# Kernel tuning notes

Hardware: AMD Instinct MI355X
Metric: run time of the kernel (lower is better)

The kernel has to match this reference:

```python
import jax, jax.numpy as jnp
import numpy as np

QMAX = 127.0  # torch.iinfo(torch.int8).max


def setup_inputs() -> dict:
    key = jax.random.key(0)
    k1, k2 = jax.random.split(key)
    input_act = jax.random.normal(k1, (4, 2048, 4096), dtype=jnp.float32)
    # nn.Linear weight: [out_features, in_features], fp weights pre-quantization
    weight = jax.random.normal(k2, (4096, 4096), dtype=jnp.float32) * 0.02
    return {"input_act": input_act, "weight": weight}


def reference(input_act, weight):
    # --- weight_quant (per-channel over in_features) ---
    w_scale = jnp.max(jnp.abs(weight), axis=-1, keepdims=True) / QMAX      # [O, 1]
    w_q = jnp.round(weight / w_scale).astype(jnp.int8)                      # int8 weight

    # --- activation quant (per-token over last dim) ---
    a_scale = jnp.max(jnp.abs(input_act), axis=-1, keepdims=True) / QMAX    # [B, S, 1]
    x_q = jnp.round(input_act / a_scale).astype(jnp.int8)                   # int8 acts

    # --- int8 GEMM with int32 accumulation (torch._int_mm semantics) ---
    # [B, S, K] @ [K, O] -> [B, S, O]
    acc = jnp.matmul(x_q.astype(jnp.int32), w_q.T.astype(jnp.int32))        # exact int32

    # --- dequant: scale = input_act_scale * weight_scale.T, then cast to fp16 ---
    scale = a_scale * w_scale.T[None, :, :]                                 # [B, S, O]
    out = (acc.astype(jnp.float32) * scale).astype(jnp.float16)
    return out
```

## Files before the change

### kernel.cpp

```cpp
#include <hip/hip_runtime.h>
#include <hip/hip_fp16.h>
#include <cstdint>

typedef int v4i __attribute__((ext_vector_type(4)));

#define AS1C(p) ((const __attribute__((address_space(1))) void*)(p))
#define AS3(p)  ((__attribute__((address_space(3))) void*)(p))

__global__ __launch_bounds__(256) void quant_fused(const float* __restrict__ X,
                                                   const float* __restrict__ W,
                                                   int8_t* __restrict__ Xq,
                                                   int8_t* __restrict__ Wq,
                                                   float* __restrict__ a_scale,
                                                   float* __restrict__ w_scale) {
    const int row = blockIdx.x;
    const float* src;
    int8_t* dst;
    float* scp;
    if (row < 8192) {
        src = X + (size_t)row * 4096;  dst = Xq + (size_t)row * 4096;  scp = a_scale + row;
    } else {
        const int r = row - 8192;
        src = W + (size_t)r * 4096;    dst = Wq + (size_t)r * 4096;    scp = w_scale + r;
    }
    const float4* xv = (const float4*)src;
    const int tid = threadIdx.x;

    float4 v[4];
#pragma unroll
    for (int j = 0; j < 4; ++j) v[j] = xv[tid * 4 + j];

    float m = 0.0f;
#pragma unroll
    for (int j = 0; j < 4; ++j) {
        m = fmaxf(m, fmaxf(fmaxf(fabsf(v[j].x), fabsf(v[j].y)),
                           fmaxf(fabsf(v[j].z), fabsf(v[j].w))));
    }
    for (int off = 32; off > 0; off >>= 1)
        m = fmaxf(m, __shfl_xor(m, off, 64));

    __shared__ float wmax[4];
    __shared__ float s_sc;
    const int lane = tid & 63;
    const int wv = tid >> 6;
    if (lane == 0) wmax[wv] = m;
    __syncthreads();
    if (tid == 0) {
        float mm = fmaxf(fmaxf(wmax[0], wmax[1]), fmaxf(wmax[2], wmax[3]));
        float sc = mm / 127.0f;
        *scp = sc;
        s_sc = sc;
    }
    __syncthreads();
    const float sc = s_sc;

    v4i qw;
#pragma unroll
    for (int j = 0; j < 4; ++j) {
        const int b0 = (int)(unsigned char)(signed char)(int)rintf(v[j].x / sc);
        const int b1 = (int)(unsigned char)(signed char)(int)rintf(v[j].y / sc);
        const int b2 = (int)(unsigned char)(signed char)(int)rintf(v[j].z / sc);
        const int b3 = (int)(signed char)(int)rintf(v[j].w / sc);
        qw[j] = b0 | (b1 << 8) | (b2 << 16) | (b3 << 24);
    }
    *(v4i*)(dst + (size_t)tid * 16) = qw;
}

__global__ __launch_bounds__(512, 2) void gemm_i8(const int8_t* __restrict__ Aq,
                                                  const int8_t* __restrict__ Bq,
                                                  const float* __restrict__ a_scale,
                                                  const float* __restrict__ w_scale,
                                                  float* __restrict__ out) {
    extern __shared__ __align__(16) int8_t smem[];

    const int K = 4096;
    const int bid = blockIdx.x;
    const int wg  = (bid & 7) * 64 + (bid >> 3);
    const int n0 = (wg & 15) * 256;
    const int m0 = (wg >> 4) * 256;

    const int tid  = threadIdx.x;
    const int lane = tid & 63;
    const int wid  = tid >> 6;
    const int wm   = wid >> 2;
    const int wn   = wid & 3;

    const int rsel  = lane & 15;
    const int kswz  = ((lane >> 4) << 4) ^ (((rsel >> 1) & 3) << 4);
    const int abase = (wm * 128 + rsel) * 64 + kswz;
    const int bbase = 16384 + (wn * 64 + rsel) * 64 + kswz;

    const int strow = tid >> 2;
    const int stswz = ((strow >> 1) & 3) << 4;
    const int stcol = ((tid & 3) << 4) ^ stswz;
    const int8_t* gA = Aq + (size_t)(m0 + strow) * K + stcol;
    const int8_t* gB = Bq + (size_t)(n0 + strow) * K + stcol;
    const size_t rstep = (size_t)128 * K;
    const int ldsst = wid * 1024;

    v4i acc[8][4] = {};
    v4i aFa[8], aFb[8], bFa[4], bFb[4];

#define STAGE(buf, kt) do {                                                          \
    int8_t* _d = smem + (buf) * 32768;                                               \
    const int8_t* _a = gA + (size_t)(kt) * 64;                                       \
    const int8_t* _b = gB + (size_t)(kt) * 64;                                       \
    __builtin_amdgcn_global_load_lds(AS1C(_a),         AS3(_d + ldsst),         16, 0, 0); \
    __builtin_amdgcn_global_load_lds(AS1C(_a + rstep), AS3(_d + 8192  + ldsst), 16, 0, 0); \
    __builtin_amdgcn_global_load_lds(AS1C(_b),         AS3(_d + 16384 + ldsst), 16, 0, 0); \
    __builtin_amdgcn_global_load_lds(AS1C(_b + rstep), AS3(_d + 24576 + ldsst), 16, 0, 0); \
  } while (0)

#define READS(g, NA, NB, gsrc, goff) do {                                            \
    NA[2*(g)]     = *(const v4i*)(bufN + abase + (2*(g))     * 1024);                \
    NA[2*(g) + 1] = *(const v4i*)(bufN + abase + (2*(g) + 1) * 1024);                \
    NB[(g)]       = *(const v4i*)(bufN + bbase + (g) * 1024);                        \
    __builtin_amdgcn_global_load_lds(AS1C(gsrc), AS3(pD + (goff) + ldsst), 16, 0, 0);\
  } while (0)

#define MFMAS(g, CA, CB) do {                                                        \
    __builtin_amdgcn_s_setprio(1);                                                   \
    _Pragma("unroll")                                                                \
    for (int nt = 0; nt < 4; ++nt) {                                                 \
        acc[2*(g)][nt] = __builtin_amdgcn_mfma_i32_16x16x64_i8(                      \
            CA[2*(g)], CB[nt], acc[2*(g)][nt], 0, 0, 0);                             \
        acc[2*(g)+1][nt] = __builtin_amdgcn_mfma_i32_16x16x64_i8(                    \
            CA[2*(g)+1], CB[nt], acc[2*(g)+1][nt], 0, 0, 0);                         \
    }                                                                                \
    __builtin_amdgcn_s_setprio(0);                                                   \
  } while (0)

#define GROUP_RW(g, CA, CB, NA, NB, gsrc, goff)  do {                                \
    READS(g, NA, NB, gsrc, goff);                                                    \
    __builtin_amdgcn_sched_barrier(0);                                               \
    MFMAS(g, CA, CB);                                                                \
    __builtin_amdgcn_sched_barrier(0);                                               \
  } while (0)

#define GROUP_WR(g, CA, CB, NA, NB, gsrc, goff)  do {                                \
    MFMAS(g, CA, CB);                                                                \
    __builtin_amdgcn_sched_barrier(0);                                               \
    READS(g, NA, NB, gsrc, goff);                                                    \
    __builtin_amdgcn_sched_barrier(0);                                               \
  } while (0)

#define KSTEP(G, u, CA, CB, NA, NB, kt4) do {                                        \
    const int kt  = (kt4) + (u);                                                     \
    const int8_t* bufN = smem + (((u) + 1) & 3) * 32768;                             \
    int8_t* pD = smem + (((u) + 3) & 3) * 32768;                                     \
    const int ktp = (kt + 3 < 64) ? (kt + 3) : 63;                                   \
    const int8_t* _a = gA + (size_t)ktp * 64;                                        \
    const int8_t* _b = gB + (size_t)ktp * 64;                                        \
    asm volatile("s_waitcnt vmcnt(4)" ::: "memory");                                 \
    __builtin_amdgcn_s_barrier();                                                    \
    __builtin_amdgcn_sched_barrier(0);                                               \
    G(0, CA, CB, NA, NB, _a,         0);                                             \
    G(1, CA, CB, NA, NB, _a + rstep, 8192);                                          \
    G(2, CA, CB, NA, NB, _b,         16384);                                         \
    G(3, CA, CB, NA, NB, _b + rstep, 24576);                                         \
  } while (0)

    STAGE(0, 0); STAGE(1, 1); STAGE(2, 2);
    asm volatile("s_waitcnt vmcnt(8)" ::: "memory");
    __builtin_amdgcn_s_barrier();
#pragma unroll
    for (int mt = 0; mt < 8; ++mt) aFa[mt] = *(const v4i*)(smem + abase + mt * 1024);
#pragma unroll
    for (int nt = 0; nt < 4; ++nt) bFa[nt] = *(const v4i*)(smem + bbase + nt * 1024);

    if (wid < 4) {
        for (int kt4 = 0; kt4 < 64; kt4 += 4) {
            KSTEP(GROUP_RW, 0, aFa, bFa, aFb, bFb, kt4);
            KSTEP(GROUP_RW, 1, aFb, bFb, aFa, bFa, kt4);
            KSTEP(GROUP_RW, 2, aFa, bFa, aFb, bFb, kt4);
            KSTEP(GROUP_RW, 3, aFb, bFb, aFa, bFa, kt4);
        }
    } else {
        for (int kt4 = 0; kt4 < 64; kt4 += 4) {
            KSTEP(GROUP_WR, 0, aFa, bFa, aFb, bFb, kt4);
            KSTEP(GROUP_WR, 1, aFb, bFb, aFa, bFa, kt4);
            KSTEP(GROUP_WR, 2, aFa, bFa, aFb, bFb, kt4);
            KSTEP(GROUP_WR, 3, aFb, bFb, aFa, bFa, kt4);
        }
    }

    const int r0  = (lane >> 4) << 2;
    const int col = lane & 15;
#pragma unroll
    for (int mt = 0; mt < 8; ++mt) {
        const int tbase = m0 + wm * 128 + mt * 16 + r0;
        float as[4];
#pragma unroll
        for (int r = 0; r < 4; ++r) as[r] = a_scale[tbase + r];
#pragma unroll
        for (int nt = 0; nt < 4; ++nt) {
            const int o = n0 + wn * 64 + nt * 16 + col;
            const float wsc = w_scale[o];
#pragma unroll
            for (int r = 0; r < 4; ++r) {
                float v = (float)acc[mt][nt][r] * as[r] * wsc;
                out[(size_t)(tbase + r) * 4096 + o] = __half2float(__float2half_rn(v));
            }
        }
    }
#undef KSTEP
#undef GROUP_RW
#undef GROUP_WR
#undef MFMAS
#undef READS
#undef STAGE
}

extern "C" void kernel_launch(void* const* d_in, const int* in_sizes, int n_in,
                              void* d_out, int out_size, void* d_ws, size_t ws_size,
                              hipStream_t stream) {
    const float* input_act = (const float*)d_in[0];
    const float* weight    = (const float*)d_in[1];
    float* out = (float*)d_out;

    const int K = 4096, O = 4096, T = 8192;

    int8_t* x_q = (int8_t*)d_ws;
    int8_t* w_q = x_q + (size_t)T * K;
    float* a_scale = (float*)(w_q + (size_t)O * K);
    float* w_scale = a_scale + T;

    static bool attr_done = false;
    if (!attr_done) {
        hipFuncSetAttribute(reinterpret_cast<const void*>(gemm_i8),
                            hipFuncAttributeMaxDynamicSharedMemorySize, 131072);
        attr_done = true;
    }

    quant_fused<<<T + O, 256, 0, stream>>>(input_act, weight, x_q, w_q,
                                           a_scale, w_scale);

    dim3 grid(512);
    gemm_i8<<<grid, 512, 131072, stream>>>(x_q, w_q, a_scale, w_scale, out);
}
```

Before: 177.0 us.

## Switch int8 GEMM inner loop from 16x16x64 to 32x32x32 MFMA

Replaces the 16x16x64 int8 MFMA tiles with 32x32x32 MFMA instructions, cutting the instruction count per K-step from 32 to 16. The LDS fragment reads are remapped to the 32-lane row layout with the existing XOR swizzle, and the epilogue is rewritten for the 16-register output layout. The larger MFMA has higher operand reuse per instruction and fewer issue slots, but it changes the LDS access pattern and bank-conflict behaviour, and its latency interacts differently with the hand-interleaved read/MFMA schedule.

```diff
diff --git a/kernel.cpp b/kernel.cpp
--- a/kernel.cpp
+++ b/kernel.cpp
@@ -2,7 +2,8 @@
 #include <hip/hip_fp16.h>
 #include <cstdint>
 
-typedef int v4i __attribute__((ext_vector_type(4)));
+typedef int v4i  __attribute__((ext_vector_type(4)));
+typedef int v16i __attribute__((ext_vector_type(16)));
 
 #define AS1C(p) ((const __attribute__((address_space(1))) void*)(p))
 #define AS3(p)  ((__attribute__((address_space(3))) void*)(p))
@@ -85,10 +86,18 @@
     const int wm   = wid >> 2;
     const int wn   = wid & 3;
 
-    const int rsel  = lane & 15;
-    const int kswz  = ((lane >> 4) << 4) ^ (((rsel >> 1) & 3) << 4);
-    const int abase = (wm * 128 + rsel) * 64 + kswz;
-    const int bbase = 16384 + (wn * 64 + rsel) * 64 + kswz;
+    const int rsel32 = lane & 31;
+    const int hi     = lane >> 5;
+    const int arow   = wm * 128 + rsel32;
+    const int brow   = wn * 64  + rsel32;
+    const int swzA   = (arow >> 1) & 3;
+    const int swzB   = (brow >> 1) & 3;
+    const int abase32 = arow * 64;
+    const int bbase32 = 16384 + brow * 64;
+    const int chA0 = ((0 + hi) ^ swzA) << 4;
+    const int chA1 = ((2 + hi) ^ swzA) << 4;
+    const int chB0 = ((0 + hi) ^ swzB) << 4;
+    const int chB1 = ((2 + hi) ^ swzB) << 4;
 
     const int strow = tid >> 2;
     const int stswz = ((strow >> 1) & 3) << 4;
@@ -98,7 +107,7 @@
     const size_t rstep = (size_t)128 * K;
     const int ldsst = wid * 1024;
 
-    v4i acc[8][4] = {};
+    v16i acc[8] = {};
     v4i aFa[8], aFb[8], bFa[4], bFb[4];
 
 #define STAGE(buf, kt) do {                                                          \
@@ -112,21 +121,23 @@
   } while (0)
 
 #define READS(g, NA, NB, gsrc, goff) do {                                            \
-    NA[2*(g)]     = *(const v4i*)(bufN + abase + (2*(g))     * 1024);                \
-    NA[2*(g) + 1] = *(const v4i*)(bufN + abase + (2*(g) + 1) * 1024);                \
-    NB[(g)]       = *(const v4i*)(bufN + bbase + (g) * 1024);                        \
+    NA[2*(g)]     = *(const v4i*)(bufN + abase32 + (g) * 2048 + chA0);               \
+    NA[2*(g) + 1] = *(const v4i*)(bufN + abase32 + (g) * 2048 + chA1);               \
+    NB[(g)]       = *(const v4i*)(bufN + bbase32 + ((g) >> 1) * 2048                 \
+                                  + (((g) & 1) ? chB1 : chB0));                      \
     __builtin_amdgcn_global_load_lds(AS1C(gsrc), AS3(pD + (goff) + ldsst), 16, 0, 0);\
   } while (0)
 
 #define MFMAS(g, CA, CB) do {                                                        \
     __builtin_amdgcn_s_setprio(1);                                                   \
-    _Pragma("unroll")                                                                \
-    for (int nt = 0; nt < 4; ++nt) {                                                 \
-        acc[2*(g)][nt] = __builtin_amdgcn_mfma_i32_16x16x64_i8(                      \
-            CA[2*(g)], CB[nt], acc[2*(g)][nt], 0, 0, 0);                             \
-        acc[2*(g)+1][nt] = __builtin_amdgcn_mfma_i32_16x16x64_i8(                    \
-            CA[2*(g)+1], CB[nt], acc[2*(g)+1][nt], 0, 0, 0);                         \
-    }                                                                                \
+    acc[2*(g)]   = __builtin_amdgcn_mfma_i32_32x32x32_i8(CA[2*(g)],   CB[0],         \
+                                                         acc[2*(g)],   0, 0, 0);    \
+    acc[2*(g)]   = __builtin_amdgcn_mfma_i32_32x32x32_i8(CA[2*(g)+1], CB[1],         \
+                                                         acc[2*(g)],   0, 0, 0);    \
+    acc[2*(g)+1] = __builtin_amdgcn_mfma_i32_32x32x32_i8(CA[2*(g)],   CB[2],         \
+                                                         acc[2*(g)+1], 0, 0, 0);    \
+    acc[2*(g)+1] = __builtin_amdgcn_mfma_i32_32x32x32_i8(CA[2*(g)+1], CB[3],         \
+                                                         acc[2*(g)+1], 0, 0, 0);    \
     __builtin_amdgcn_s_setprio(0);                                                   \
   } while (0)
 
@@ -164,9 +175,12 @@
     asm volatile("s_waitcnt vmcnt(8)" ::: "memory");
     __builtin_amdgcn_s_barrier();
 #pragma unroll
-    for (int mt = 0; mt < 8; ++mt) aFa[mt] = *(const v4i*)(smem + abase + mt * 1024);
-#pragma unroll
-    for (int nt = 0; nt < 4; ++nt) bFa[nt] = *(const v4i*)(smem + bbase + nt * 1024);
+    for (int g = 0; g < 4; ++g) {
+        aFa[2*g]     = *(const v4i*)(smem + abase32 + g * 2048 + chA0);
+        aFa[2*g + 1] = *(const v4i*)(smem + abase32 + g * 2048 + chA1);
+        bFa[g]       = *(const v4i*)(smem + bbase32 + (g >> 1) * 2048
+                                     + ((g & 1) ? chB1 : chB0));
+    }
 
     if (wid < 4) {
         for (int kt4 = 0; kt4 < 64; kt4 += 4) {
@@ -184,22 +198,25 @@
         }
     }
 
-    const int r0  = (lane >> 4) << 2;
-    const int col = lane & 15;
-#pragma unroll
-    for (int mt = 0; mt < 8; ++mt) {
-        const int tbase = m0 + wm * 128 + mt * 16 + r0;
-        float as[4];
-#pragma unroll
-        for (int r = 0; r < 4; ++r) as[r] = a_scale[tbase + r];
-#pragma unroll
-        for (int nt = 0; nt < 4; ++nt) {
-            const int o = n0 + wn * 64 + nt * 16 + col;
+#pragma unroll
+    for (int rb = 0; rb < 4; ++rb) {
+        const int tbase = m0 + wm * 128 + rb * 32;
+        float as[16];
+#pragma unroll
+        for (int q = 0; q < 4; ++q)
+#pragma unroll
+            for (int j = 0; j < 4; ++j)
+                as[q * 4 + j] = a_scale[tbase + 8 * q + 4 * hi + j];
+#pragma unroll
+        for (int cb = 0; cb < 2; ++cb) {
+            const int o = n0 + wn * 64 + cb * 32 + rsel32;
             const float wsc = w_scale[o];
-#pragma unroll
-            for (int r = 0; r < 4; ++r) {
-                float v = (float)acc[mt][nt][r] * as[r] * wsc;
-                out[(size_t)(tbase + r) * 4096 + o] = __half2float(__float2half_rn(v));
+            const v16i a16 = acc[rb * 2 + cb];
+#pragma unroll
+            for (int reg = 0; reg < 16; ++reg) {
+                const int row = tbase + (reg & 3) + 8 * (reg >> 2) + 4 * hi;
+                float v = (float)a16[reg] * as[reg] * wsc;
+                out[(size_t)row * 4096 + o] = __half2float(__float2half_rn(v));
             }
         }
     }
```

Measured after the change: 193.3 us. +9.2%, slower.
